# Performance work log

Measured on AMD Instinct MI355X. Metric: run time of the kernel, lower is better.

Reference implementation:

```python
import jax, jax.numpy as jnp
import numpy as np

B, S, D_IN, D_OUT = 4, 2048, 1024, 1024


def setup_inputs() -> dict:
    key = jax.random.key(0)
    ks = jax.random.split(key, 7)
    s_in = 1.0 / np.sqrt(D_IN)
    return {
        "x": jax.random.normal(ks[0], (B, S, D_IN), dtype=jnp.float32),
        "Wq": jax.random.uniform(ks[1], (D_IN, D_OUT), jnp.float32, -s_in, s_in),
        "bq": jax.random.uniform(ks[2], (D_OUT,), jnp.float32, -s_in, s_in),
        "Wk": jax.random.uniform(ks[3], (D_IN, D_OUT), jnp.float32, -s_in, s_in),
        "bk": jax.random.uniform(ks[4], (D_OUT,), jnp.float32, -s_in, s_in),
        "Wv": jax.random.uniform(ks[5], (D_IN, D_OUT), jnp.float32, -s_in, s_in),
        "bv": jax.random.uniform(ks[6], (D_OUT,), jnp.float32, -s_in, s_in),
    }


def reference(x, Wq, bq, Wk, bk, Wv, bv):
    # q,k,v: [B, S, D_OUT]
    q = jnp.einsum("bsd,de->bse", x, Wq) + bq
    k = jnp.einsum("bsd,de->bse", x, Wk) + bk
    v = jnp.einsum("bsd,de->bse", x, Wv) + bv
    scale = 1.0 / jnp.sqrt(jnp.asarray(q.shape[-1], q.dtype))
    scores = jnp.einsum("bqe,bke->bqk", q, k) * scale  # [B, S, S]
    attn = jax.nn.softmax(scores, axis=-1)
    return jnp.einsum("bqk,bke->bqe", attn, v)
```

## Files before the change

### kernel.cpp

```cpp
#include <hip/hip_runtime.h>
#include <hip/hip_bf16.h>
#include <stdint.h>


#define Bsz 4
#define Ssz 2048
#define Dsz 1024

typedef __attribute__((ext_vector_type(8))) short short8;
typedef __attribute__((ext_vector_type(4))) float floatx4;
typedef const __attribute__((address_space(1))) void* gptr_t;
typedef __attribute__((address_space(3))) void* lptr_t;

__device__ __forceinline__ ushort f32_to_bf16(float f) {
    union { float f; uint32_t u; } c; c.f = f;
    uint32_t u = c.u;
    u += 0x7fffu + ((u >> 16) & 1u);
    return (ushort)(u >> 16);
}

__global__ __launch_bounds__(256, 2) void k_qkv(
    const ushort* __restrict__ xb, const ushort* __restrict__ Wt,
    const float* __restrict__ bq, const float* __restrict__ bk,
    const float* __restrict__ bv, ushort* __restrict__ QKV,
    ushort* __restrict__ Vt)
{
    __shared__ __align__(16) ushort smem[32768];

    const int tid  = threadIdx.x;
    const int bx   = blockIdx.x;
    const int by   = blockIdx.y;
    const int row0 = by * 128;
    const int col0 = bx * 128;

    const int lane = tid & 63;
    const int wave = tid >> 6;
    const int wr   = (wave >> 1) * 64;
    const int wc   = (wave & 1) * 64;
    const int m16  = lane & 15;
    const int quad = lane >> 4;

    floatx4 acc[3][4][4];
#pragma unroll
    for (int z = 0; z < 3; z++)
#pragma unroll
        for (int i = 0; i < 4; i++)
#pragma unroll
            for (int j = 0; j < 4; j++) acc[z][i][j] = (floatx4){0.f, 0.f, 0.f, 0.f};

    const int srow = tid >> 2;
    const int skc  = (tid & 3) ^ ((srow >> 1) & 3);
    const ushort* ga = xb + (size_t)(row0 + srow) * Dsz + skc * 8;
    const ushort* gb0 = Wt + (size_t)(col0 + srow) * Dsz + skc * 8;

    const int aoff = (quad ^ ((m16 >> 1) & 3)) * 8;

#define LSA(buf) (smem + (buf) * 4096)
#define LSB(buf, z) (smem + 8192 + ((buf) * 3 + (z)) * 4096)

    __builtin_amdgcn_global_load_lds((gptr_t)(ga),                    (lptr_t)(LSA(0) + tid * 8),        16, 0, 0);
    __builtin_amdgcn_global_load_lds((gptr_t)(ga + (size_t)64 * Dsz), (lptr_t)(LSA(0) + 2048 + tid * 8), 16, 0, 0);
#pragma unroll
    for (int z = 0; z < 3; z++) {
        const ushort* gb = gb0 + (size_t)z * Dsz * Dsz;
        __builtin_amdgcn_global_load_lds((gptr_t)(gb),                    (lptr_t)(LSB(0, z) + tid * 8),        16, 0, 0);
        __builtin_amdgcn_global_load_lds((gptr_t)(gb + (size_t)64 * Dsz), (lptr_t)(LSB(0, z) + 2048 + tid * 8), 16, 0, 0);
    }

    for (int k0 = 0; k0 < Dsz; k0 += 32) {
        const int cur = (k0 >> 5) & 1;
        __syncthreads();
        if (k0 + 32 < Dsz) {
            const int nxt = cur ^ 1;
            const int kn = k0 + 32;
            __builtin_amdgcn_global_load_lds((gptr_t)(ga + kn),                    (lptr_t)(LSA(nxt) + tid * 8),        16, 0, 0);
            __builtin_amdgcn_global_load_lds((gptr_t)(ga + kn + (size_t)64 * Dsz), (lptr_t)(LSA(nxt) + 2048 + tid * 8), 16, 0, 0);
#pragma unroll
            for (int z = 0; z < 3; z++) {
                const ushort* gb = gb0 + (size_t)z * Dsz * Dsz + kn;
                __builtin_amdgcn_global_load_lds((gptr_t)(gb),                    (lptr_t)(LSB(nxt, z) + tid * 8),        16, 0, 0);
                __builtin_amdgcn_global_load_lds((gptr_t)(gb + (size_t)64 * Dsz), (lptr_t)(LSB(nxt, z) + 2048 + tid * 8), 16, 0, 0);
            }
        }

        short8 af[4];
#pragma unroll
        for (int mi = 0; mi < 4; mi++)
            af[mi] = *(const short8*)(LSA(cur) + (wr + mi * 16 + m16) * 32 + aoff);
#pragma unroll
        for (int z = 0; z < 3; z++) {
            short8 bfr[4];
#pragma unroll
            for (int ni = 0; ni < 4; ni++)
                bfr[ni] = *(const short8*)(LSB(cur, z) + (wc + ni * 16 + m16) * 32 + aoff);
#pragma unroll
            for (int mi = 0; mi < 4; mi++)
#pragma unroll
                for (int ni = 0; ni < 4; ni++)
                    acc[z][mi][ni] = __builtin_amdgcn_mfma_f32_16x16x32_bf16(af[mi], bfr[ni], acc[z][mi][ni], 0, 0, 0);
        }
    }

#pragma unroll
    for (int ni = 0; ni < 4; ni++) {
        const int gcol = col0 + wc + ni * 16 + m16;
        const float bqv = bq[gcol], bkv = bk[gcol];
#pragma unroll
        for (int mi = 0; mi < 4; mi++) {
            const int grow0 = row0 + wr + mi * 16 + quad * 4;
#pragma unroll
            for (int j = 0; j < 4; j++) {
                QKV[(size_t)(grow0 + j) * Dsz + gcol] = f32_to_bf16((acc[0][mi][ni][j] + bqv) * 0.03125f);
                QKV[(size_t)(Bsz * Ssz) * Dsz + (size_t)(grow0 + j) * Dsz + gcol] = f32_to_bf16(acc[1][mi][ni][j] + bkv);
            }
        }
    }

    __syncthreads();
#pragma unroll
    for (int ni = 0; ni < 4; ni++) {
        const int e_l = wc + ni * 16 + m16;
        const float bvv = bv[col0 + e_l];
#pragma unroll
        for (int mi = 0; mi < 4; mi++) {
            const int s_l = wr + mi * 16 + quad * 4;
            ushort4 vp;
            vp.x = f32_to_bf16(acc[2][mi][ni][0] + bvv);
            vp.y = f32_to_bf16(acc[2][mi][ni][1] + bvv);
            vp.z = f32_to_bf16(acc[2][mi][ni][2] + bvv);
            vp.w = f32_to_bf16(acc[2][mi][ni][3] + bvv);
            *(ushort4*)&smem[e_l * 136 + s_l] = vp;
        }
    }
    __syncthreads();
    const int batch = by >> 4;
    const int sbase = (by & 15) * 128;
    ushort* vout = Vt + (size_t)batch * Dsz * Ssz + sbase;
#pragma unroll
    for (int pass = 0; pass < 8; pass++) {
        const int e_l = pass * 16 + (tid >> 4);
        const int ss  = (tid & 15) * 8;
        short8 v = *(const short8*)&smem[e_l * 136 + ss];
        *(short8*)&vout[(size_t)(col0 + e_l) * Ssz + ss] = v;
    }
#undef LSA
#undef LSB
}

template <bool OUT_BF16>
__device__ __forceinline__ void gemm128(
    int bx, int by,
    const ushort* __restrict__ A, int lda,
    const ushort* __restrict__ Bt, int ldb,
    int K,
    void* __restrict__ Cout, int ldc,
    const float* __restrict__ bias, float alpha)
{
    __shared__ ushort lsA[2][128 * 32];
    __shared__ ushort lsB[2][128 * 32];

    const int tid  = threadIdx.x;
    const int row0 = by * 128;
    const int col0 = bx * 128;

    const int lane = tid & 63;
    const int wave = tid >> 6;
    const int wr   = (wave >> 1) * 64;
    const int wc   = (wave & 1) * 64;
    const int m16  = lane & 15;
    const int quad = lane >> 4;

    floatx4 acc[4][4];
#pragma unroll
    for (int i = 0; i < 4; i++)
#pragma unroll
        for (int j = 0; j < 4; j++) acc[i][j] = (floatx4){0.f, 0.f, 0.f, 0.f};

    const int srow = tid >> 2;
    const int skc  = (tid & 3) ^ ((srow >> 1) & 3);
    const ushort* ga = A  + (size_t)(row0 + srow) * lda + skc * 8;
    const ushort* gb = Bt + (size_t)(col0 + srow) * ldb + skc * 8;
    const int aoff = (quad ^ ((m16 >> 1) & 3)) * 8;

    __builtin_amdgcn_global_load_lds((gptr_t)(ga),                     (lptr_t)(lsA[0] + tid * 8),        16, 0, 0);
    __builtin_amdgcn_global_load_lds((gptr_t)(ga + (size_t)64 * lda), (lptr_t)(lsA[0] + 2048 + tid * 8), 16, 0, 0);
    __builtin_amdgcn_global_load_lds((gptr_t)(gb),                     (lptr_t)(lsB[0] + tid * 8),        16, 0, 0);
    __builtin_amdgcn_global_load_lds((gptr_t)(gb + (size_t)64 * ldb), (lptr_t)(lsB[0] + 2048 + tid * 8), 16, 0, 0);

    for (int k0 = 0; k0 < K; k0 += 32) {
        const int cur = (k0 >> 5) & 1;
        __syncthreads();
        if (k0 + 32 < K) {
            const int nxt = cur ^ 1;
            const int kn = k0 + 32;
            __builtin_amdgcn_global_load_lds((gptr_t)(ga + kn),                     (lptr_t)(lsA[nxt] + tid * 8),        16, 0, 0);
            __builtin_amdgcn_global_load_lds((gptr_t)(ga + kn + (size_t)64 * lda), (lptr_t)(lsA[nxt] + 2048 + tid * 8), 16, 0, 0);
            __builtin_amdgcn_global_load_lds((gptr_t)(gb + kn),                     (lptr_t)(lsB[nxt] + tid * 8),        16, 0, 0);
            __builtin_amdgcn_global_load_lds((gptr_t)(gb + kn + (size_t)64 * ldb), (lptr_t)(lsB[nxt] + 2048 + tid * 8), 16, 0, 0);
        }

        short8 af[4], bfr[4];
#pragma unroll
        for (int mi = 0; mi < 4; mi++)
            af[mi] = *(const short8*)&lsA[cur][(wr + mi * 16 + m16) * 32 + aoff];
#pragma unroll
        for (int ni = 0; ni < 4; ni++)
            bfr[ni] = *(const short8*)&lsB[cur][(wc + ni * 16 + m16) * 32 + aoff];
#pragma unroll
        for (int mi = 0; mi < 4; mi++)
#pragma unroll
            for (int ni = 0; ni < 4; ni++)
                acc[mi][ni] = __builtin_amdgcn_mfma_f32_16x16x32_bf16(af[mi], bfr[ni], acc[mi][ni], 0, 0, 0);
    }

#pragma unroll
    for (int ni = 0; ni < 4; ni++) {
        const int gcol = col0 + wc + ni * 16 + m16;
        const float bv = bias ? bias[gcol] : 0.0f;
#pragma unroll
        for (int mi = 0; mi < 4; mi++) {
            const int grow0 = row0 + wr + mi * 16 + quad * 4;
#pragma unroll
            for (int j = 0; j < 4; j++) {
                float v = (acc[mi][ni][j] + bv) * alpha;
                if (OUT_BF16)
                    ((ushort*)Cout)[(size_t)(grow0 + j) * ldc + gcol] = f32_to_bf16(v);
                else
                    ((float*)Cout)[(size_t)(grow0 + j) * ldc + gcol] = v;
            }
        }
    }
}

__global__ __launch_bounds__(256) void k_prep(
    const float* __restrict__ x, ushort* __restrict__ xb,
    const float* __restrict__ Wq, const float* __restrict__ Wk,
    const float* __restrict__ Wv, ushort* __restrict__ Wt)
{
    __shared__ float tile[32][33];
    const int bid = blockIdx.x;
    const int tid = threadIdx.x;
    if (bid < 8192) {
        int i = (bid * 256 + tid) * 4;
        float4 v = *(const float4*)(x + i);
        ushort4 o;
        o.x = f32_to_bf16(v.x); o.y = f32_to_bf16(v.y);
        o.z = f32_to_bf16(v.z); o.w = f32_to_bf16(v.w);
        *(ushort4*)(xb + i) = o;
    } else {
        const int wb = bid - 8192;
        const int z  = wb >> 10;
        const int r  = wb & 1023;
        const int nb = (r & 31) * 32;
        const int kb = (r >> 5) * 32;
        const float* W = (z == 0) ? Wq : ((z == 1) ? Wk : Wv);
        ushort* out = Wt + (size_t)z * Dsz * Dsz;
        const int tx = tid & 31, ty = tid >> 5;
#pragma unroll
        for (int j = 0; j < 32; j += 8)
            tile[ty + j][tx] = W[(size_t)(kb + ty + j) * Dsz + nb + tx];
        __syncthreads();
#pragma unroll
        for (int j = 0; j < 32; j += 8)
            out[(size_t)(nb + ty + j) * Dsz + kb + tx] = f32_to_bf16(tile[tx][ty + j]);
    }
}

__global__ __launch_bounds__(256) void k_scores(const ushort* __restrict__ QKV, float* __restrict__ scores) {
    const int b = blockIdx.z;
    const int lin = blockIdx.y * 16 + blockIdx.x;
    const int c = lin & 7, m = lin >> 3;
    const int by = 2 * c + (m & 1);
    const int bx = m >> 1;
    const ushort* Q = QKV + (size_t)b * Ssz * Dsz;
    const ushort* Kb = QKV + (size_t)(Bsz + b) * Ssz * Dsz;
    gemm128<false>(bx, by, Q, Dsz, Kb, Dsz, Dsz, scores + (size_t)b * Ssz * Ssz, Ssz, nullptr, 1.0f);
}

__global__ __launch_bounds__(256) void k_softmax(float* __restrict__ scores) {
    const size_t row = blockIdx.x;
    float* rp = scores + row * Ssz;
    const int tid = threadIdx.x;
    float4 v0 = ((const float4*)rp)[tid];
    float4 v1 = ((const float4*)rp)[tid + 256];
    float m = fmaxf(fmaxf(fmaxf(v0.x, v0.y), fmaxf(v0.z, v0.w)),
                    fmaxf(fmaxf(v1.x, v1.y), fmaxf(v1.z, v1.w)));
#pragma unroll
    for (int o = 32; o > 0; o >>= 1) m = fmaxf(m, __shfl_down(m, o, 64));
    __shared__ float redm[4];
    if ((tid & 63) == 0) redm[tid >> 6] = m;
    __syncthreads();
    const float rm = fmaxf(fmaxf(redm[0], redm[1]), fmaxf(redm[2], redm[3]));
    v0.x = __expf(v0.x - rm); v0.y = __expf(v0.y - rm);
    v0.z = __expf(v0.z - rm); v0.w = __expf(v0.w - rm);
    v1.x = __expf(v1.x - rm); v1.y = __expf(v1.y - rm);
    v1.z = __expf(v1.z - rm); v1.w = __expf(v1.w - rm);
    float s = v0.x + v0.y + v0.z + v0.w + v1.x + v1.y + v1.z + v1.w;
#pragma unroll
    for (int o = 32; o > 0; o >>= 1) s += __shfl_down(s, o, 64);
    __shared__ float reds[4];
    if ((tid & 63) == 0) reds[tid >> 6] = s;
    __syncthreads();
    const float inv = 1.0f / (reds[0] + reds[1] + reds[2] + reds[3]);
    ushort4 o0, o1;
    o0.x = f32_to_bf16(v0.x * inv); o0.y = f32_to_bf16(v0.y * inv);
    o0.z = f32_to_bf16(v0.z * inv); o0.w = f32_to_bf16(v0.w * inv);
    o1.x = f32_to_bf16(v1.x * inv); o1.y = f32_to_bf16(v1.y * inv);
    o1.z = f32_to_bf16(v1.z * inv); o1.w = f32_to_bf16(v1.w * inv);
    ((ushort4*)rp)[tid] = o0;
    ((ushort4*)rp)[tid + 256] = o1;
}

__global__ __launch_bounds__(256) void k_pv(const float* __restrict__ scores, const ushort* __restrict__ Vt,
                                            float* __restrict__ out) {
    const int b = blockIdx.z;
    const int lin = blockIdx.y * 8 + blockIdx.x;
    const int c = lin & 7, m = lin >> 3;
    const int by = 2 * c + (m & 1);
    const int bx = m >> 1;
    const ushort* P = (const ushort*)(scores + (size_t)b * Ssz * Ssz);
    const ushort* Bt = Vt + (size_t)b * Dsz * Ssz;
    gemm128<false>(bx, by, P, 2 * Ssz, Bt, Ssz, Ssz, out + (size_t)b * Ssz * Dsz, Dsz, nullptr, 1.0f);
}

extern "C" void kernel_launch(void* const* d_in, const int* in_sizes, int n_in,
                              void* d_out, int out_size, void* d_ws, size_t ws_size,
                              hipStream_t stream) {
    const float* x  = (const float*)d_in[0];
    const float* Wq = (const float*)d_in[1];
    const float* bq = (const float*)d_in[2];
    const float* Wk = (const float*)d_in[3];
    const float* bk = (const float*)d_in[4];
    const float* Wv = (const float*)d_in[5];
    const float* bv = (const float*)d_in[6];
    float* out = (float*)d_out;

    char* ws = (char*)d_ws;
    ushort* xb     = (ushort*)(ws);
    ushort* Wt     = (ushort*)(ws + 16777216);
    ushort* QKV    = (ushort*)(ws + 23068672);
    ushort* Vt     = (ushort*)(ws + 73400320);
    float*  scores = (float*) (ws + 90177536);

    k_prep<<<dim3(8192 + 3072), dim3(256), 0, stream>>>(x, xb, Wq, Wk, Wv, Wt);
    k_qkv<<<dim3(Dsz / 128, Bsz * Ssz / 128), dim3(256), 0, stream>>>(xb, Wt, bq, bk, bv, QKV, Vt);
    k_scores<<<dim3(Ssz / 128, Ssz / 128, Bsz), dim3(256), 0, stream>>>(QKV, scores);
    k_softmax<<<dim3(Bsz * Ssz), dim3(256), 0, stream>>>(scores);
    k_pv<<<dim3(Dsz / 128, Ssz / 128, Bsz), dim3(256), 0, stream>>>(scores, Vt, out);
}
```

Baseline: 274.5 us.

## Use 128x256 tiles with 512-thread blocks for scores and PV GEMMs

Replaces the 128x128 GEMM helper with a 128x256 tile run by 8 waves (512 threads), which halves A-tile reloads per output. It also remaps block indices into a 1D grid with a custom swizzle for L2 locality. The scores grid drops to 512 blocks and the PV grid to 256 blocks. That is about one block per CU on PV, so occupancy and tail balance may suffer.

```diff
diff --git a/kernel.cpp b/kernel.cpp
--- a/kernel.cpp
+++ b/kernel.cpp
@@ -147,26 +147,21 @@
 #undef LSB
 }
 
-template <bool OUT_BF16>
-__device__ __forceinline__ void gemm128(
-    int bx, int by,
+__device__ __forceinline__ void gemm128x256(
+    int row0, int col0,
     const ushort* __restrict__ A, int lda,
     const ushort* __restrict__ Bt, int ldb,
     int K,
-    void* __restrict__ Cout, int ldc,
-    const float* __restrict__ bias, float alpha)
+    float* __restrict__ Cout, int ldc)
 {
     __shared__ ushort lsA[2][128 * 32];
-    __shared__ ushort lsB[2][128 * 32];
+    __shared__ ushort lsB[2][256 * 32];
 
     const int tid  = threadIdx.x;
-    const int row0 = by * 128;
-    const int col0 = bx * 128;
-
     const int lane = tid & 63;
     const int wave = tid >> 6;
-    const int wr   = (wave >> 1) * 64;
-    const int wc   = (wave & 1) * 64;
+    const int wr   = (wave >> 2) * 64;
+    const int wc   = (wave & 3) * 64;
     const int m16  = lane & 15;
     const int quad = lane >> 4;
 
@@ -182,10 +177,9 @@
     const ushort* gb = Bt + (size_t)(col0 + srow) * ldb + skc * 8;
     const int aoff = (quad ^ ((m16 >> 1) & 3)) * 8;
 
-    __builtin_amdgcn_global_load_lds((gptr_t)(ga),                     (lptr_t)(lsA[0] + tid * 8),        16, 0, 0);
-    __builtin_amdgcn_global_load_lds((gptr_t)(ga + (size_t)64 * lda), (lptr_t)(lsA[0] + 2048 + tid * 8), 16, 0, 0);
-    __builtin_amdgcn_global_load_lds((gptr_t)(gb),                     (lptr_t)(lsB[0] + tid * 8),        16, 0, 0);
-    __builtin_amdgcn_global_load_lds((gptr_t)(gb + (size_t)64 * ldb), (lptr_t)(lsB[0] + 2048 + tid * 8), 16, 0, 0);
+    __builtin_amdgcn_global_load_lds((gptr_t)(ga),                      (lptr_t)(lsA[0] + tid * 8),        16, 0, 0);
+    __builtin_amdgcn_global_load_lds((gptr_t)(gb),                      (lptr_t)(lsB[0] + tid * 8),        16, 0, 0);
+    __builtin_amdgcn_global_load_lds((gptr_t)(gb + (size_t)128 * ldb),  (lptr_t)(lsB[0] + 4096 + tid * 8), 16, 0, 0);
 
     for (int k0 = 0; k0 < K; k0 += 32) {
         const int cur = (k0 >> 5) & 1;
@@ -193,10 +187,9 @@
         if (k0 + 32 < K) {
             const int nxt = cur ^ 1;
             const int kn = k0 + 32;
-            __builtin_amdgcn_global_load_lds((gptr_t)(ga + kn),                     (lptr_t)(lsA[nxt] + tid * 8),        16, 0, 0);
-            __builtin_amdgcn_global_load_lds((gptr_t)(ga + kn + (size_t)64 * lda), (lptr_t)(lsA[nxt] + 2048 + tid * 8), 16, 0, 0);
-            __builtin_amdgcn_global_load_lds((gptr_t)(gb + kn),                     (lptr_t)(lsB[nxt] + tid * 8),        16, 0, 0);
-            __builtin_amdgcn_global_load_lds((gptr_t)(gb + kn + (size_t)64 * ldb), (lptr_t)(lsB[nxt] + 2048 + tid * 8), 16, 0, 0);
+            __builtin_amdgcn_global_load_lds((gptr_t)(ga + kn),                      (lptr_t)(lsA[nxt] + tid * 8),        16, 0, 0);
+            __builtin_amdgcn_global_load_lds((gptr_t)(gb + kn),                      (lptr_t)(lsB[nxt] + tid * 8),        16, 0, 0);
+            __builtin_amdgcn_global_load_lds((gptr_t)(gb + kn + (size_t)128 * ldb),  (lptr_t)(lsB[nxt] + 4096 + tid * 8), 16, 0, 0);
         }
 
         short8 af[4], bfr[4];
@@ -216,18 +209,12 @@
 #pragma unroll
     for (int ni = 0; ni < 4; ni++) {
         const int gcol = col0 + wc + ni * 16 + m16;
-        const float bv = bias ? bias[gcol] : 0.0f;
 #pragma unroll
         for (int mi = 0; mi < 4; mi++) {
             const int grow0 = row0 + wr + mi * 16 + quad * 4;
 #pragma unroll
-            for (int j = 0; j < 4; j++) {
-                float v = (acc[mi][ni][j] + bv) * alpha;
-                if (OUT_BF16)
-                    ((ushort*)Cout)[(size_t)(grow0 + j) * ldc + gcol] = f32_to_bf16(v);
-                else
-                    ((float*)Cout)[(size_t)(grow0 + j) * ldc + gcol] = v;
-            }
+            for (int j = 0; j < 4; j++)
+                Cout[(size_t)(grow0 + j) * ldc + gcol] = acc[mi][ni][j];
         }
     }
 }
@@ -266,15 +253,16 @@
     }
 }
 
-__global__ __launch_bounds__(256) void k_scores(const ushort* __restrict__ QKV, float* __restrict__ scores) {
-    const int b = blockIdx.z;
-    const int lin = blockIdx.y * 16 + blockIdx.x;
-    const int c = lin & 7, m = lin >> 3;
-    const int by = 2 * c + (m & 1);
-    const int bx = m >> 1;
-    const ushort* Q = QKV + (size_t)b * Ssz * Dsz;
+__global__ __launch_bounds__(512, 1) void k_scores(const ushort* __restrict__ QKV, float* __restrict__ scores) {
+    const int bid = blockIdx.x;
+    const int bn  = bid & 7;
+    const int i   = bid >> 3;
+    const int bm  = i & 15;
+    const int b   = i >> 4;
+    const ushort* Q  = QKV + (size_t)b * Ssz * Dsz;
     const ushort* Kb = QKV + (size_t)(Bsz + b) * Ssz * Dsz;
-    gemm128<false>(bx, by, Q, Dsz, Kb, Dsz, Dsz, scores + (size_t)b * Ssz * Ssz, Ssz, nullptr, 1.0f);
+    gemm128x256(bm * 128, bn * 256, Q, Dsz, Kb, Dsz, Dsz,
+                scores + (size_t)b * Ssz * Ssz, Ssz);
 }
 
 __global__ __launch_bounds__(256) void k_softmax(float* __restrict__ scores) {
@@ -311,16 +299,19 @@
     ((ushort4*)rp)[tid + 256] = o1;
 }
 
-__global__ __launch_bounds__(256) void k_pv(const float* __restrict__ scores, const ushort* __restrict__ Vt,
-                                            float* __restrict__ out) {
-    const int b = blockIdx.z;
-    const int lin = blockIdx.y * 8 + blockIdx.x;
-    const int c = lin & 7, m = lin >> 3;
-    const int by = 2 * c + (m & 1);
-    const int bx = m >> 1;
-    const ushort* P = (const ushort*)(scores + (size_t)b * Ssz * Ssz);
+__global__ __launch_bounds__(512, 1) void k_pv(const float* __restrict__ scores, const ushort* __restrict__ Vt,
+                                               float* __restrict__ out) {
+    const int bid = blockIdx.x;
+    const int c   = bid & 7;
+    const int i   = bid >> 3;
+    const int bx  = i & 3;
+    const int sid = c * 8 + (i >> 2);
+    const int by  = sid & 15;
+    const int b   = sid >> 4;
+    const ushort* P  = (const ushort*)(scores + (size_t)b * Ssz * Ssz);
     const ushort* Bt = Vt + (size_t)b * Dsz * Ssz;
-    gemm128<false>(bx, by, P, 2 * Ssz, Bt, Ssz, Ssz, out + (size_t)b * Ssz * Dsz, Dsz, nullptr, 1.0f);
+    gemm128x256(by * 128, bx * 256, P, 2 * Ssz, Bt, Ssz, Ssz,
+                out + (size_t)b * Ssz * Dsz, Dsz);
 }
 
 extern "C" void kernel_launch(void* const* d_in, const int* in_sizes, int n_in,
@@ -344,7 +335,7 @@
 
     k_prep<<<dim3(8192 + 3072), dim3(256), 0, stream>>>(x, xb, Wq, Wk, Wv, Wt);
     k_qkv<<<dim3(Dsz / 128, Bsz * Ssz / 128), dim3(256), 0, stream>>>(xb, Wt, bq, bk, bv, QKV, Vt);
-    k_scores<<<dim3(Ssz / 128, Ssz / 128, Bsz), dim3(256), 0, stream>>>(QKV, scores);
+    k_scores<<<dim3(512), dim3(512), 0, stream>>>(QKV, scores);
     k_softmax<<<dim3(Bsz * Ssz), dim3(256), 0, stream>>>(scores);
-    k_pv<<<dim3(Dsz / 128, Ssz / 128, Bsz), dim3(256), 0, stream>>>(scores, Vt, out);
-}
+    k_pv<<<dim3(256), dim3(512), 0, stream>>>(scores, Vt, out);
+}
```

After: 263.7 us. -3.9%, faster.
